# Kernel tuning notes

Measured on AMD Instinct MI355X. Metric: run time of the kernel, lower is better.

The kernel has to match this reference:

```python
import jax, jax.numpy as jnp
import numpy as np
import math

NUM_CLASSES = 722
BLUR_RANGE = 3
# gaussian_val(dist, sigma=1) = exp(-2**dist / (2 * 2**1)) = exp(-2**dist / 4)
DECAYS = [math.exp(-(2.0 ** d) / 4.0) for d in range(BLUR_RANGE + 1)]


def setup_inputs() -> dict:
    key = jax.random.key(0)
    k1, k2 = jax.random.split(key)
    pred = jax.random.normal(k1, (32, 2048, NUM_CLASSES), dtype=jnp.float32)
    target = jax.random.randint(k2, (32, 2048), 0, NUM_CLASSES, dtype=jnp.int32)
    return {"pred": pred, "target": target}


def _smoothed_label(target):
    # target: (b, t) int -> (b, t, C) float32 gaussian-blurred one-hot.
    b, t = target.shape
    bi = jnp.arange(b)[:, None]   # (b, 1)
    ti = jnp.arange(t)[None, :]   # (1, t)
    one_hot = jnp.zeros((b, t, NUM_CLASSES), dtype=jnp.float32)
    # Same scatter order as the torch loop: dist = blur..0, direction +1 then -1;
    # later (smaller-dist) scatters overwrite earlier ones, incl. clamped indices.
    for dist in range(BLUR_RANGE, -1, -1):
        for direction in (1, -1):
            blur_idx = jnp.clip(target + direction * dist, 0, NUM_CLASSES - 1)
            one_hot = one_hot.at[bi, ti, blur_idx].set(DECAYS[dist])
    # to_onehot: exact target position gets 1.0 (overwrites decay[0]).
    one_hot = one_hot.at[bi, ti, target].set(1.0)
    return one_hot


def reference(pred, target):
    # pred: (b, t, C) logits; target: (b, t) class indices.
    pred_logit = jax.nn.log_softmax(pred, axis=-1)
    target_smoothed = _smoothed_label(target)
    target_loss_sum = jnp.sum(-pred_logit * target_smoothed, axis=-1)  # (b, t)
    return jnp.mean(target_loss_sum)
```

## Files before the change

kernel.cpp:

```cpp
#include <hip/hip_runtime.h>
#include <math.h>

#define NC 722
#define NF2 361
#define NROWS 65536
#define ROWS_PER_WAVE 4
#define WAVES_PER_BLOCK 4
#define ROWS_PER_BLOCK 16
#define KITERS 6
#define NBLOCKS (NROWS / ROWS_PER_BLOCK)

__global__ __launch_bounds__(256) void ce_gauss_kernel(
        const float* __restrict__ pred,
        const int* __restrict__ target,
        float* __restrict__ partials) {
    const int lane = threadIdx.x & 63;
    const int wave = threadIdx.x >> 6;
    __shared__ float wave_sums[WAVES_PER_BLOCK];

    const int row0 = blockIdx.x * ROWS_PER_BLOCK + wave * ROWS_PER_WAVE;

    const float2* __restrict__ p2[ROWS_PER_WAVE];
    #pragma unroll
    for (int rr = 0; rr < ROWS_PER_WAVE; ++rr)
        p2[rr] = (const float2*)(pred + (size_t)(row0 + rr) * NC);

    float2 v[ROWS_PER_WAVE][KITERS];
    #pragma unroll
    for (int k = 0; k < KITERS; ++k) {
        int idx = lane + (k << 6);
        if (idx > NF2 - 1) idx = NF2 - 1;
        #pragma unroll
        for (int rr = 0; rr < ROWS_PER_WAVE; ++rr)
            v[rr][k] = p2[rr][idx];
    }

    int t0 = target[row0 + 0];
    int t1 = target[row0 + 1];
    int t2 = target[row0 + 2];
    int t3 = target[row0 + 3];

    float se[ROWS_PER_WAVE] = {0.f, 0.f, 0.f, 0.f};
    #pragma unroll
    for (int k = 0; k < KITERS; ++k) {
        const bool valid = (k < KITERS - 1) || (lane < NF2 - 5 * 64);
        #pragma unroll
        for (int rr = 0; rr < ROWS_PER_WAVE; ++rr) {
            const float s = __expf(v[rr][k].x) + __expf(v[rr][k].y);
            se[rr] += valid ? s : 0.f;
        }
    }

    #pragma unroll
    for (int rr = 0; rr < ROWS_PER_WAVE; ++rr) {
        #pragma unroll
        for (int off = 32; off > 0; off >>= 1)
            se[rr] += __shfl_xor(se[rr], off, 64);
    }

    const int grr = lane >> 3;
    const int gj  = lane & 7;
    const float se_sel = (grr & 2) ? ((grr & 1) ? se[3] : se[2])
                                   : ((grr & 1) ? se[1] : se[0]);
    const int   t_sel  = (grr & 2) ? ((grr & 1) ? t3 : t2)
                                   : ((grr & 1) ? t1 : t0);
    int ad = gj - 3; ad = (ad < 0) ? -ad : ad;
    const float w = (ad == 0) ? 1.0f
                  : (ad == 1) ? 0.606530659713f
                  : (ad == 2) ? 0.367879441171f
                  : (ad == 3) ? 0.135335283237f
                  : 0.0f;
    const int c = t_sel - 3 + gj;
    const bool tap_valid = (grr < ROWS_PER_WAVE) & (gj < 7) &
                           (c >= 0) & (c <= NC - 1);
    int cc = c; if (cc < 0) cc = 0; if (cc > NC - 1) cc = NC - 1;
    const float pv = pred[(size_t)(row0 + (grr & 3)) * NC + cc];
    const float lse = __logf(se_sel);
    float contrib = tap_valid ? (w * (lse - pv)) : 0.f;

    #pragma unroll
    for (int off = 32; off > 0; off >>= 1)
        contrib += __shfl_xor(contrib, off, 64);

    if (lane == 0) wave_sums[wave] = contrib;
    __syncthreads();
    if (threadIdx.x == 0) {
        partials[blockIdx.x] =
            wave_sums[0] + wave_sums[1] + wave_sums[2] + wave_sums[3];
    }
}

__global__ __launch_bounds__(256) void reduce_partials_kernel(
        const float* __restrict__ partials, float* __restrict__ out) {
    const int lane = threadIdx.x & 63;
    const int wave = threadIdx.x >> 6;
    __shared__ float ws[4];

    float s = 0.f;
    #pragma unroll
    for (int k = 0; k < NBLOCKS / 256; ++k)
        s += partials[threadIdx.x + (k << 8)];
    #pragma unroll
    for (int off = 32; off > 0; off >>= 1)
        s += __shfl_xor(s, off, 64);
    if (lane == 0) ws[wave] = s;
    __syncthreads();
    if (threadIdx.x == 0)
        out[0] = (ws[0] + ws[1] + ws[2] + ws[3]) * (1.0f / (float)NROWS);
}

extern "C" void kernel_launch(void* const* d_in, const int* in_sizes, int n_in,
                              void* d_out, int out_size, void* d_ws, size_t ws_size,
                              hipStream_t stream) {
    const float* pred = (const float*)d_in[0];
    const int* target = (const int*)d_in[1];
    float* out = (float*)d_out;
    float* partials = (float*)d_ws;

    ce_gauss_kernel<<<NBLOCKS, 256, 0, stream>>>(pred, target, partials);
    reduce_partials_kernel<<<1, 256, 0, stream>>>(partials, out);
}
```

Baseline: 254.4 us.

## Load row pairs with float4 and process eight rows per wave

Each wave now handles eight rows, treated as four contiguous row pairs. Each pair spans 1444 floats, which is 16-byte aligned, so it is read with float4 loads, and the boundary float4 is split between the two rows' exp sums. This widens memory transactions and gives every lane of the 64-lane gather phase a real tap. In exchange each thread holds twice as many registers for loaded values, and the grid has half as many blocks.

```diff
diff --git a/kernel.cpp b/kernel.cpp
--- a/kernel.cpp
+++ b/kernel.cpp
@@ -2,11 +2,12 @@
 #include <math.h>
 
 #define NC 722
-#define NF2 361
 #define NROWS 65536
-#define ROWS_PER_WAVE 4
+#define PAIRS_PER_WAVE 4
+#define ROWS_PER_WAVE 8
 #define WAVES_PER_BLOCK 4
-#define ROWS_PER_BLOCK 16
+#define ROWS_PER_BLOCK 32
+#define NF4 361
 #define KITERS 6
 #define NBLOCKS (NROWS / ROWS_PER_BLOCK)
 
@@ -20,35 +21,49 @@
 
     const int row0 = blockIdx.x * ROWS_PER_BLOCK + wave * ROWS_PER_WAVE;
 
-    const float2* __restrict__ p2[ROWS_PER_WAVE];
+    const float4* __restrict__ p4[PAIRS_PER_WAVE];
     #pragma unroll
-    for (int rr = 0; rr < ROWS_PER_WAVE; ++rr)
-        p2[rr] = (const float2*)(pred + (size_t)(row0 + rr) * NC);
+    for (int p = 0; p < PAIRS_PER_WAVE; ++p)
+        p4[p] = (const float4*)(pred + (size_t)(row0 + 2 * p) * NC);
 
-    float2 v[ROWS_PER_WAVE][KITERS];
+    float4 v[PAIRS_PER_WAVE][KITERS];
     #pragma unroll
     for (int k = 0; k < KITERS; ++k) {
-        int idx = lane + (k << 6);
-        if (idx > NF2 - 1) idx = NF2 - 1;
+        int g = lane + (k << 6);
+        if (g > NF4 - 1) g = NF4 - 1;
         #pragma unroll
-        for (int rr = 0; rr < ROWS_PER_WAVE; ++rr)
-            v[rr][k] = p2[rr][idx];
+        for (int p = 0; p < PAIRS_PER_WAVE; ++p)
+            v[p][k] = p4[p][g];
     }
 
-    int t0 = target[row0 + 0];
-    int t1 = target[row0 + 1];
-    int t2 = target[row0 + 2];
-    int t3 = target[row0 + 3];
+    const int t0 = target[row0 + 0], t1 = target[row0 + 1];
+    const int t2 = target[row0 + 2], t3 = target[row0 + 3];
+    const int t4 = target[row0 + 4], t5 = target[row0 + 5];
+    const int t6 = target[row0 + 6], t7 = target[row0 + 7];
 
-    float se[ROWS_PER_WAVE] = {0.f, 0.f, 0.f, 0.f};
+    float se[ROWS_PER_WAVE] = {0.f,0.f,0.f,0.f,0.f,0.f,0.f,0.f};
     #pragma unroll
-    for (int k = 0; k < KITERS; ++k) {
-        const bool valid = (k < KITERS - 1) || (lane < NF2 - 5 * 64);
+    for (int p = 0; p < PAIRS_PER_WAVE; ++p) {
+        float sa = 0.f, sb = 0.f;
         #pragma unroll
-        for (int rr = 0; rr < ROWS_PER_WAVE; ++rr) {
-            const float s = __expf(v[rr][k].x) + __expf(v[rr][k].y);
-            se[rr] += valid ? s : 0.f;
+        for (int k = 0; k < KITERS; ++k) {
+            const float4 q = v[p][k];
+            const float e0 = __expf(q.x), e1 = __expf(q.y);
+            const float e2 = __expf(q.z), e3 = __expf(q.w);
+            const float sxy = e0 + e1, szw = e2 + e3, s4 = sxy + szw;
+            if (k <= 1) {
+                sa += s4;
+            } else if (k >= 3) {
+                const bool valid = (k < 5) || (lane < 41);
+                sb += valid ? s4 : 0.f;
+            } else {
+                const int g = 128 + lane;
+                sa += (g < 180) ? s4 : ((g == 180) ? sxy : 0.f);
+                sb += (g > 180) ? s4 : ((g == 180) ? szw : 0.f);
+            }
         }
+        se[2 * p]     = sa;
+        se[2 * p + 1] = sb;
     }
 
     #pragma unroll
@@ -60,10 +75,21 @@
 
     const int grr = lane >> 3;
     const int gj  = lane & 7;
-    const float se_sel = (grr & 2) ? ((grr & 1) ? se[3] : se[2])
-                                   : ((grr & 1) ? se[1] : se[0]);
-    const int   t_sel  = (grr & 2) ? ((grr & 1) ? t3 : t2)
-                                   : ((grr & 1) ? t1 : t0);
+    const float s01 = (grr & 1) ? se[1] : se[0];
+    const float s23 = (grr & 1) ? se[3] : se[2];
+    const float s45 = (grr & 1) ? se[5] : se[4];
+    const float s67 = (grr & 1) ? se[7] : se[6];
+    const float s0123 = (grr & 2) ? s23 : s01;
+    const float s4567 = (grr & 2) ? s67 : s45;
+    const float se_sel = (grr & 4) ? s4567 : s0123;
+    const int u01 = (grr & 1) ? t1 : t0;
+    const int u23 = (grr & 1) ? t3 : t2;
+    const int u45 = (grr & 1) ? t5 : t4;
+    const int u67 = (grr & 1) ? t7 : t6;
+    const int u0123 = (grr & 2) ? u23 : u01;
+    const int u4567 = (grr & 2) ? u67 : u45;
+    const int t_sel = (grr & 4) ? u4567 : u0123;
+
     int ad = gj - 3; ad = (ad < 0) ? -ad : ad;
     const float w = (ad == 0) ? 1.0f
                   : (ad == 1) ? 0.606530659713f
@@ -71,10 +97,9 @@
                   : (ad == 3) ? 0.135335283237f
                   : 0.0f;
     const int c = t_sel - 3 + gj;
-    const bool tap_valid = (grr < ROWS_PER_WAVE) & (gj < 7) &
-                           (c >= 0) & (c <= NC - 1);
+    const bool tap_valid = (gj < 7) & (c >= 0) & (c <= NC - 1);
     int cc = c; if (cc < 0) cc = 0; if (cc > NC - 1) cc = NC - 1;
-    const float pv = pred[(size_t)(row0 + (grr & 3)) * NC + cc];
+    const float pv = pred[(size_t)(row0 + grr) * NC + cc];
     const float lse = __logf(se_sel);
     float contrib = tap_valid ? (w * (lse - pv)) : 0.f;
 
```

After: 258.2 us. About the same (+1.5%).
